# Kernel tuning notes

Measured on AMD Instinct MI355X. Metric: run time of the kernel, lower is better.

## Reference

```python
import jax, jax.numpy as jnp
import numpy as np

N_NODES = 20000
N_EDGES = 320000
N_GRAPHS = 16
NEG_SLOPE = 0.2


def gat_layer(x, src, dst, W, al, ar, b):
    # x: [N, F_in]; W: [F_in, H*D]; al/ar: [H, D]; b: [H*D]
    H, D = al.shape
    N = x.shape[0]
    f = (x @ W).reshape(N, H, D)                      # projected features [N,H,D]
    el = jnp.sum(f * al[None], axis=-1)                # [N,H]
    er = jnp.sum(f * ar[None], axis=-1)                # [N,H]
    e = jax.nn.leaky_relu(el[src] + er[dst], NEG_SLOPE)  # [E,H]
    # numerically stable segment softmax over incoming edges of each dst node
    m = jax.ops.segment_max(e, dst, num_segments=N)    # [N,H]
    m = jnp.where(jnp.isfinite(m), m, 0.0)
    ex = jnp.exp(e - m[dst])                           # [E,H]
    denom = jax.ops.segment_sum(ex, dst, num_segments=N)  # [N,H]
    msg = ex[:, :, None] * f[src]                      # [E,H,D]
    num = jax.ops.segment_sum(msg, dst, num_segments=N)   # [N,H,D]
    rst = num / jnp.where(denom > 0, denom, 1.0)[:, :, None]
    return rst + b.reshape(1, H, D)


def setup_inputs() -> dict:
    key = jax.random.key(0)
    ks = jax.random.split(key, 16)
    in_dim, hid, H = 128, 128, 3
    x = jax.random.normal(ks[0], (N_NODES, in_dim), dtype=jnp.float32)
    src = jax.random.randint(ks[1], (N_EDGES,), 0, N_NODES, dtype=jnp.int32)
    dst = jax.random.randint(ks[2], (N_EDGES,), 0, N_NODES, dtype=jnp.int32)
    graph_ids = jnp.sort(jax.random.randint(ks[3], (N_NODES,), 0, N_GRAPHS, dtype=jnp.int32))
    s = lambda d: 1.0 / np.sqrt(d)
    W1 = jax.random.normal(ks[4], (in_dim, H * hid), jnp.float32) * s(in_dim)
    al1 = jax.random.normal(ks[5], (H, hid), jnp.float32) * s(hid)
    ar1 = jax.random.normal(ks[6], (H, hid), jnp.float32) * s(hid)
    b1 = jnp.zeros((H * hid,), jnp.float32)
    W2 = jax.random.normal(ks[7], (H * hid, hid), jnp.float32) * s(H * hid)
    al2 = jax.random.normal(ks[8], (1, hid), jnp.float32) * s(hid)
    ar2 = jax.random.normal(ks[9], (1, hid), jnp.float32) * s(hid)
    b2 = jnp.zeros((hid,), jnp.float32)
    linW = jax.random.normal(ks[10], (hid, hid), jnp.float32) * s(hid)
    linb = jnp.zeros((hid,), jnp.float32)
    return dict(x=x, src=src, dst=dst, graph_ids=graph_ids, W1=W1, al1=al1,
                ar1=ar1, b1=b1, W2=W2, al2=al2, ar2=ar2, b2=b2, linW=linW, linb=linb)


def reference(x, src, dst, graph_ids, W1, al1, ar1, b1, W2, al2, ar2, b2, linW, linb):
    h = gat_layer(x, src, dst, W1, al1, ar1, b1)       # [N,3,hid]
    h = jax.nn.elu(h.reshape(h.shape[0], -1))          # [N,3*hid]
    h = gat_layer(h, src, dst, W2, al2, ar2, b2)       # [N,1,hid]
    h = h.squeeze(1)                                   # [N,hid]
    # dgl.mean_nodes over batched graph
    sums = jax.ops.segment_sum(h, graph_ids, num_segments=N_GRAPHS)      # [G,hid]
    cnts = jax.ops.segment_sum(jnp.ones_like(graph_ids, jnp.float32), graph_ids, num_segments=N_GRAPHS)
    hg = sums / jnp.maximum(cnts, 1.0)[:, None]
    return jax.nn.relu(hg @ linW + linb)
```

## Files before the change

kernel.cpp:

```cpp
#include <hip/hip_runtime.h>
#include <hip/hip_bf16.h>

#define NN 20000
#define NE 320000
#define NG 16
#define PSPLIT 32


__global__ void hist_kernel(const int* __restrict__ dst, int* __restrict__ indeg, int E) {
  int e = blockIdx.x * 256 + threadIdx.x;
  if (e < E) atomicAdd(&indeg[dst[e]], 1);
}

__global__ void exscan_kernel(const int* __restrict__ in, int* __restrict__ outp, int n) {
  __shared__ int wsum[16];
  __shared__ int wexcl[16];
  __shared__ int tot_s;
  __shared__ int carry_s;
  int t = threadIdx.x;
  int lane = t & 63, wv = t >> 6;
  if (t == 0) carry_s = 0;
  __syncthreads();
  for (int base = 0; base < n; base += 1024) {
    int i = base + t;
    int v = (i < n) ? in[i] : 0;
    int x = v;
#pragma unroll
    for (int off = 1; off < 64; off <<= 1) {
      int y = __shfl_up(x, off);
      if (lane >= off) x += y;
    }
    if (lane == 63) wsum[wv] = x;
    __syncthreads();
    int carry = carry_s;
    if (t < 16) {
      int s = wsum[t];
      int xs = s;
#pragma unroll
      for (int off = 1; off < 16; off <<= 1) {
        int y = __shfl_up(xs, off);
        if (t >= off) xs += y;
      }
      wexcl[t] = xs - s;
      if (t == 15) tot_s = xs;
    }
    __syncthreads();
    if (i < n) outp[i] = carry + wexcl[wv] + (x - v);
    if (t == 0) carry_s = carry + tot_s;
  }
  if (t == 0) outp[n] = carry_s;
}

__global__ void scatter_kernel(const int* __restrict__ src, const int* __restrict__ dst,
                               const int* __restrict__ rowptr, int* __restrict__ cursor,
                               int* __restrict__ csr_src, int E) {
  int e = blockIdx.x * 256 + threadIdx.x;
  if (e < E) {
    int d = dst[e];
    int p = atomicAdd(&cursor[d], 1);
    csr_src[rowptr[d] + p] = src[e];
  }
}


template <int K, int NFULL>
__launch_bounds__(256)
__global__ void gemm64_kernel(const float* __restrict__ A, const float* __restrict__ B,
                              float* __restrict__ C, int M) {
  __shared__ float As[64 * 36];
  __shared__ float Bs[32 * 128];
  int t = threadIdx.x;
  int m0 = blockIdx.x * 64;
  int n0 = blockIdx.y * 128;
  int tm = t >> 4, tn = t & 15;
  float acc[4][8];
#pragma unroll
  for (int i = 0; i < 4; i++)
#pragma unroll
    for (int j = 0; j < 8; j++) acc[i][j] = 0.f;

  for (int k0 = 0; k0 < K; k0 += 32) {
#pragma unroll
    for (int i = 0; i < 2; i++) {
      int idx = t + i * 256;
      int r = idx >> 3, kq = (idx & 7) * 4;
      int gm = m0 + r;
      float4 v = make_float4(0.f, 0.f, 0.f, 0.f);
      if (gm < M) v = *(const float4*)&A[(size_t)gm * K + k0 + kq];
      *(float4*)&As[r * 36 + kq] = v;
    }
#pragma unroll
    for (int i = 0; i < 4; i++) {
      int idx = t + i * 256;
      int kk = idx >> 5, nq = (idx & 31) * 4;
      float4 v = *(const float4*)&B[(size_t)(k0 + kk) * NFULL + n0 + nq];
      *(float4*)&Bs[kk * 128 + nq] = v;
    }
    __syncthreads();
#pragma unroll 8
    for (int k = 0; k < 32; k++) {
      float af[4];
#pragma unroll
      for (int i = 0; i < 4; i++) af[i] = As[(tm * 4 + i) * 36 + k];
      float4 b0 = *(const float4*)&Bs[k * 128 + tn * 4];
      float4 b1 = *(const float4*)&Bs[k * 128 + 64 + tn * 4];
      float bf[8] = {b0.x, b0.y, b0.z, b0.w, b1.x, b1.y, b1.z, b1.w};
#pragma unroll
      for (int i = 0; i < 4; i++)
#pragma unroll
        for (int j = 0; j < 8; j++) acc[i][j] += af[i] * bf[j];
    }
    __syncthreads();
  }
#pragma unroll
  for (int i = 0; i < 4; i++) {
    int gm = m0 + tm * 4 + i;
    if (gm < M) {
      *(float4*)&C[(size_t)gm * NFULL + n0 + tn * 4] =
          make_float4(acc[i][0], acc[i][1], acc[i][2], acc[i][3]);
      *(float4*)&C[(size_t)gm * NFULL + n0 + 64 + tn * 4] =
          make_float4(acc[i][4], acc[i][5], acc[i][6], acc[i][7]);
    }
  }
}


__global__ void att_coef_kernel(const float* __restrict__ f, const float* __restrict__ al,
                                const float* __restrict__ ar, float* __restrict__ el,
                                float* __restrict__ er, int NH, int H) {
  int w = (blockIdx.x * 256 + threadIdx.x) >> 6;
  int lane = threadIdx.x & 63;
  if (w >= NH) return;
  int h = w % H;
  const float* fr = f + (size_t)w * 128;
  float v0 = fr[lane], v1 = fr[64 + lane];
  float a0 = al[h * 128 + lane], a1 = al[h * 128 + 64 + lane];
  float r0 = ar[h * 128 + lane], r1 = ar[h * 128 + 64 + lane];
  float se = v0 * a0 + v1 * a1;
  float sr = v0 * r0 + v1 * r1;
  for (int off = 32; off; off >>= 1) {
    se += __shfl_down(se, off);
    sr += __shfl_down(sr, off);
  }
  if (lane == 0) { el[w] = se; er[w] = sr; }
}


__global__ void aggregate3_kernel(const float* __restrict__ f, const float* __restrict__ el,
                                  const float* __restrict__ er, const float* __restrict__ bias,
                                  const int* __restrict__ rowptr, const int* __restrict__ csr_src,
                                  float* __restrict__ out) {
  int n = blockIdx.x;
  int t = threadIdx.x;
  __shared__ float wbuf[3][128];
  __shared__ int sbuf[128];
  __shared__ float red[6];
  int rs = rowptr[n];
  int deg = rowptr[n + 1] - rs;
  float er0 = er[n * 3 + 0], er1 = er[n * 3 + 1], er2 = er[n * 3 + 2];
  float psum0 = 0.f, psum1 = 0.f, psum2 = 0.f;
  int h = t >> 5;
  int d = (t & 31) * 4;
  const float* fh = f + h * 128 + d;
  float4 acc = make_float4(0.f, 0.f, 0.f, 0.f);
  for (int base = 0; base < deg; base += 128) {
    int cnt = min(128, deg - base);
    if (t < cnt) {
      int s = csr_src[rs + base + t];
      sbuf[t] = s;
      float e0 = el[s * 3 + 0] + er0, e1 = el[s * 3 + 1] + er1, e2 = el[s * 3 + 2] + er2;
      e0 = e0 > 0.f ? e0 : 0.2f * e0;
      e1 = e1 > 0.f ? e1 : 0.2f * e1;
      e2 = e2 > 0.f ? e2 : 0.2f * e2;
      float w0 = __expf(e0), w1 = __expf(e1), w2 = __expf(e2);
      wbuf[0][t] = w0; wbuf[1][t] = w1; wbuf[2][t] = w2;
      psum0 += w0; psum1 += w1; psum2 += w2;
    }
    __syncthreads();
    if (t < 96) {
      int j = 0;
      for (; j + 4 <= cnt; j += 4) {
        int s0 = sbuf[j], s1 = sbuf[j + 1], s2 = sbuf[j + 2], s3 = sbuf[j + 3];
        float4 v0 = *(const float4*)(fh + (size_t)s0 * 384);
        float4 v1 = *(const float4*)(fh + (size_t)s1 * 384);
        float4 v2 = *(const float4*)(fh + (size_t)s2 * 384);
        float4 v3 = *(const float4*)(fh + (size_t)s3 * 384);
        float w0 = wbuf[h][j], w1 = wbuf[h][j + 1], w2 = wbuf[h][j + 2], w3 = wbuf[h][j + 3];
        acc.x += w0 * v0.x + w1 * v1.x + w2 * v2.x + w3 * v3.x;
        acc.y += w0 * v0.y + w1 * v1.y + w2 * v2.y + w3 * v3.y;
        acc.z += w0 * v0.z + w1 * v1.z + w2 * v2.z + w3 * v3.z;
        acc.w += w0 * v0.w + w1 * v1.w + w2 * v2.w + w3 * v3.w;
      }
      for (; j < cnt; j++) {
        int s = sbuf[j];
        float4 v = *(const float4*)(fh + (size_t)s * 384);
        float w = wbuf[h][j];
        acc.x += w * v.x; acc.y += w * v.y; acc.z += w * v.z; acc.w += w * v.w;
      }
    }
    __syncthreads();
  }
  for (int off = 32; off; off >>= 1) {
    psum0 += __shfl_down(psum0, off);
    psum1 += __shfl_down(psum1, off);
    psum2 += __shfl_down(psum2, off);
  }
  int wv = t >> 6, ln = t & 63;
  if (ln == 0) { red[wv * 3 + 0] = psum0; red[wv * 3 + 1] = psum1; red[wv * 3 + 2] = psum2; }
  __syncthreads();
  if (t < 96) {
    float dn = red[h] + red[3 + h];
    float inv = dn > 0.f ? 1.f / dn : 0.f;
    const float* bp = bias + h * 128 + d;
    float4 r;
    r.x = acc.x * inv + bp[0];
    r.y = acc.y * inv + bp[1];
    r.z = acc.z * inv + bp[2];
    r.w = acc.w * inv + bp[3];
    r.x = r.x > 0.f ? r.x : expm1f(r.x);
    r.y = r.y > 0.f ? r.y : expm1f(r.y);
    r.z = r.z > 0.f ? r.z : expm1f(r.z);
    r.w = r.w > 0.f ? r.w : expm1f(r.w);
    *(float4*)&out[(size_t)n * 384 + h * 128 + d] = r;
  }
}


__global__ void aggregate1_kernel(const float* __restrict__ f, const float* __restrict__ el,
                                  const float* __restrict__ er, const float* __restrict__ bias,
                                  const int* __restrict__ rowptr, const int* __restrict__ csr_src,
                                  float* __restrict__ out) {
  int n = blockIdx.x;
  int t = threadIdx.x;
  __shared__ float wbuf[128];
  __shared__ int sbuf[128];
  __shared__ float red[2];
  __shared__ float4 accbuf[4][32];
  int rs = rowptr[n];
  int deg = rowptr[n + 1] - rs;
  float ern = er[n];
  float psum = 0.f;
  int g = t >> 5;
  int d = (t & 31) * 4;
  const float* fd = f + d;
  float4 acc = make_float4(0.f, 0.f, 0.f, 0.f);
  for (int base = 0; base < deg; base += 128) {
    int cnt = min(128, deg - base);
    if (t < cnt) {
      int s = csr_src[rs + base + t];
      sbuf[t] = s;
      float e = el[s] + ern;
      e = e > 0.f ? e : 0.2f * e;
      float w = __expf(e);
      wbuf[t] = w;
      psum += w;
    }
    __syncthreads();
    int j = g;
    for (; j + 4 < cnt; j += 8) {
      int s0 = sbuf[j], s1 = sbuf[j + 4];
      float4 v0 = *(const float4*)(fd + (size_t)s0 * 128);
      float4 v1 = *(const float4*)(fd + (size_t)s1 * 128);
      float w0 = wbuf[j], w1 = wbuf[j + 4];
      acc.x += w0 * v0.x + w1 * v1.x;
      acc.y += w0 * v0.y + w1 * v1.y;
      acc.z += w0 * v0.z + w1 * v1.z;
      acc.w += w0 * v0.w + w1 * v1.w;
    }
    for (; j < cnt; j += 4) {
      int s = sbuf[j];
      float4 v = *(const float4*)(fd + (size_t)s * 128);
      float w = wbuf[j];
      acc.x += w * v.x; acc.y += w * v.y; acc.z += w * v.z; acc.w += w * v.w;
    }
    __syncthreads();
  }
  for (int off = 32; off; off >>= 1) psum += __shfl_down(psum, off);
  int wv = t >> 6, ln = t & 63;
  if (ln == 0) red[wv] = psum;
  accbuf[g][t & 31] = acc;
  __syncthreads();
  if (t < 32) {
    float4 a0 = accbuf[0][t], a1 = accbuf[1][t], a2 = accbuf[2][t], a3 = accbuf[3][t];
    float dn = red[0] + red[1];
    float inv = dn > 0.f ? 1.f / dn : 0.f;
    const float* bp = bias + t * 4;
    float4 r;
    r.x = (a0.x + a1.x + a2.x + a3.x) * inv + bp[0];
    r.y = (a0.y + a1.y + a2.y + a3.y) * inv + bp[1];
    r.z = (a0.z + a1.z + a2.z + a3.z) * inv + bp[2];
    r.w = (a0.w + a1.w + a2.w + a3.w) * inv + bp[3];
    *(float4*)&out[(size_t)n * 128 + t * 4] = r;
  }
}


__global__ void pool_partial_kernel(const float* __restrict__ h2, const int* __restrict__ gid,
                                    float* __restrict__ sums, int N) {
  int g = blockIdx.x / PSPLIT;
  int sp = blockIdx.x % PSPLIT;
  int tid = threadIdx.x;
  int lo0 = 0, hi0 = N;
  while (lo0 < hi0) { int m = (lo0 + hi0) >> 1; if (gid[m] < g) lo0 = m + 1; else hi0 = m; }
  int lo1 = lo0, hi1 = N;
  while (lo1 < hi1) { int m = (lo1 + hi1) >> 1; if (gid[m] < g + 1) lo1 = m + 1; else hi1 = m; }
  float a0 = 0.f, a1 = 0.f, a2 = 0.f, a3 = 0.f;
  int n = lo0 + sp;
  for (; n + 3 * PSPLIT < lo1; n += 4 * PSPLIT) {
    a0 += h2[(size_t)n * 128 + tid];
    a1 += h2[(size_t)(n + PSPLIT) * 128 + tid];
    a2 += h2[(size_t)(n + 2 * PSPLIT) * 128 + tid];
    a3 += h2[(size_t)(n + 3 * PSPLIT) * 128 + tid];
  }
  for (; n < lo1; n += PSPLIT) a0 += h2[(size_t)n * 128 + tid];
  float acc = (a0 + a1) + (a2 + a3);
  atomicAdd(&sums[g * 128 + tid], acc);
}

__global__ void pool_final_kernel(const float* __restrict__ sums, const int* __restrict__ gid,
                                  const float* __restrict__ linW, const float* __restrict__ linb,
                                  float* __restrict__ out, int N) {
  int g = blockIdx.x;
  int tid = threadIdx.x;
  int lo0 = 0, hi0 = N;
  while (lo0 < hi0) { int m = (lo0 + hi0) >> 1; if (gid[m] < g) lo0 = m + 1; else hi0 = m; }
  int lo1 = lo0, hi1 = N;
  while (lo1 < hi1) { int m = (lo1 + hi1) >> 1; if (gid[m] < g + 1) lo1 = m + 1; else hi1 = m; }
  int cnt = lo1 - lo0;
  float hg = sums[g * 128 + tid] / (float)(cnt > 0 ? cnt : 1);
  __shared__ float hgs[128];
  hgs[tid] = hg;
  __syncthreads();
  float o = linb[tid];
#pragma unroll 4
  for (int dd = 0; dd < 128; dd++) o += hgs[dd] * linW[dd * 128 + tid];
  out[g * 128 + tid] = fmaxf(o, 0.f);
}


extern "C" void kernel_launch(void* const* d_in, const int* in_sizes, int n_in,
                              void* d_out, int out_size, void* d_ws, size_t ws_size,
                              hipStream_t stream) {
  const float* x    = (const float*)d_in[0];
  const int*   src  = (const int*)d_in[1];
  const int*   dst  = (const int*)d_in[2];
  const int*   gid  = (const int*)d_in[3];
  const float* W1   = (const float*)d_in[4];
  const float* al1  = (const float*)d_in[5];
  const float* ar1  = (const float*)d_in[6];
  const float* b1   = (const float*)d_in[7];
  const float* W2   = (const float*)d_in[8];
  const float* al2  = (const float*)d_in[9];
  const float* ar2  = (const float*)d_in[10];
  const float* b2   = (const float*)d_in[11];
  const float* linW = (const float*)d_in[12];
  const float* linb = (const float*)d_in[13];
  float* out = (float*)d_out;

  char* ws = (char*)d_ws;
  size_t off = 0;
  auto alloc = [&](size_t bytes) -> void* {
    void* p = ws + off;
    off += (bytes + 255) & ~(size_t)255;
    return p;
  };
  float* f1      = (float*)alloc((size_t)NN * 384 * 4);
  float* h1      = (float*)alloc((size_t)NN * 384 * 4);
  float* f2      = (float*)alloc((size_t)NN * 128 * 4);
  float* h2      = (float*)alloc((size_t)NN * 128 * 4);
  float* el1     = (float*)alloc((size_t)NN * 3 * 4);
  float* er1     = (float*)alloc((size_t)NN * 3 * 4);
  float* el2     = (float*)alloc((size_t)NN * 4);
  float* er2     = (float*)alloc((size_t)NN * 4);
  int*   indeg   = (int*)alloc((size_t)NN * 4);
  int*   rowptr  = (int*)alloc((size_t)(NN + 1) * 4);
  int*   cursor  = (int*)alloc((size_t)NN * 4);
  int*   csr_src = (int*)alloc((size_t)NE * 4);
  float* gsums   = (float*)alloc((size_t)NG * 128 * 4);
  (void)ws_size;

  hipMemsetAsync(indeg, 0, (size_t)NN * 4, stream);
  hipMemsetAsync(cursor, 0, (size_t)NN * 4, stream);
  hipMemsetAsync(gsums, 0, (size_t)NG * 128 * 4, stream);

  hist_kernel<<<(NE + 255) / 256, 256, 0, stream>>>(dst, indeg, NE);
  exscan_kernel<<<1, 1024, 0, stream>>>(indeg, rowptr, NN);
  scatter_kernel<<<(NE + 255) / 256, 256, 0, stream>>>(src, dst, rowptr, cursor, csr_src, NE);

  gemm64_kernel<128, 384><<<dim3(313, 3), 256, 0, stream>>>(x, W1, f1, NN);
  att_coef_kernel<<<(NN * 3 + 3) / 4, 256, 0, stream>>>(f1, al1, ar1, el1, er1, NN * 3, 3);
  aggregate3_kernel<<<NN, 128, 0, stream>>>(f1, el1, er1, b1, rowptr, csr_src, h1);

  gemm64_kernel<384, 128><<<dim3(313, 1), 256, 0, stream>>>(h1, W2, f2, NN);
  att_coef_kernel<<<(NN + 3) / 4, 256, 0, stream>>>(f2, al2, ar2, el2, er2, NN, 1);
  aggregate1_kernel<<<NN, 128, 0, stream>>>(f2, el2, er2, b2, rowptr, csr_src, h2);

  pool_partial_kernel<<<NG * PSPLIT, 128, 0, stream>>>(h2, gid, gsums, NN);
  pool_final_kernel<<<NG, 128, 0, stream>>>(gsums, gid, linW, linb, out, NN);
}
```

Measured before the change: 340.1 us.

## Aggregate raw inputs before projection in first GAT layer via linearity

Layer one no longer gathers the projected 384-wide features per edge. It computes attention logits directly from x using precomputed W1·al and W1·ar vectors. It then aggregates the 128-wide raw x per head with softmax weights and applies W1 per head afterwards, with bias and ELU fused into the GEMM epilogue. This cuts per-edge gather traffic from 384 to 128 floats per edge and drops the f1 buffer and the first att_coef pass, at the cost of writing a 384-wide aggregated buffer and a batched per-head GEMM. The three memsets are also merged into one by reordering the workspace.

Result: faster. 316.0 us (-7.1%).

```diff
diff --git a/kernel.cpp b/kernel.cpp
--- a/kernel.cpp
+++ b/kernel.cpp
@@ -63,106 +63,61 @@
 }
 
 
-template <int K, int NFULL>
-__launch_bounds__(256)
-__global__ void gemm64_kernel(const float* __restrict__ A, const float* __restrict__ B,
-                              float* __restrict__ C, int M) {
-  __shared__ float As[64 * 36];
-  __shared__ float Bs[32 * 128];
+__global__ void prep_wlr_kernel(const float* __restrict__ W1, const float* __restrict__ al1,
+                                const float* __restrict__ ar1, float* __restrict__ wlr) {
+  int t = blockIdx.x * 256 + threadIdx.x;
+  if (t >= 768) return;
+  int k = t & 127;
+  int j = t >> 7;
+  int h = j % 3;
+  const float* av = (j < 3 ? al1 : ar1) + h * 128;
+  const float* wrow = W1 + (size_t)k * 384 + h * 128;
+  float s = 0.f;
+#pragma unroll 4
+  for (int d = 0; d < 128; d++) s += wrow[d] * av[d];
+  wlr[j * 128 + k] = s;
+}
+
+__global__ void elr_kernel(const float* __restrict__ x, const float* __restrict__ wlr,
+                           float* __restrict__ el, float* __restrict__ er, int N) {
+  __shared__ float wl_s[768];
   int t = threadIdx.x;
-  int m0 = blockIdx.x * 64;
-  int n0 = blockIdx.y * 128;
-  int tm = t >> 4, tn = t & 15;
-  float acc[4][8];
-#pragma unroll
-  for (int i = 0; i < 4; i++)
-#pragma unroll
-    for (int j = 0; j < 8; j++) acc[i][j] = 0.f;
-
-  for (int k0 = 0; k0 < K; k0 += 32) {
-#pragma unroll
-    for (int i = 0; i < 2; i++) {
-      int idx = t + i * 256;
-      int r = idx >> 3, kq = (idx & 7) * 4;
-      int gm = m0 + r;
-      float4 v = make_float4(0.f, 0.f, 0.f, 0.f);
-      if (gm < M) v = *(const float4*)&A[(size_t)gm * K + k0 + kq];
-      *(float4*)&As[r * 36 + kq] = v;
-    }
-#pragma unroll
-    for (int i = 0; i < 4; i++) {
-      int idx = t + i * 256;
-      int kk = idx >> 5, nq = (idx & 31) * 4;
-      float4 v = *(const float4*)&B[(size_t)(k0 + kk) * NFULL + n0 + nq];
-      *(float4*)&Bs[kk * 128 + nq] = v;
-    }
-    __syncthreads();
-#pragma unroll 8
-    for (int k = 0; k < 32; k++) {
-      float af[4];
-#pragma unroll
-      for (int i = 0; i < 4; i++) af[i] = As[(tm * 4 + i) * 36 + k];
-      float4 b0 = *(const float4*)&Bs[k * 128 + tn * 4];
-      float4 b1 = *(const float4*)&Bs[k * 128 + 64 + tn * 4];
-      float bf[8] = {b0.x, b0.y, b0.z, b0.w, b1.x, b1.y, b1.z, b1.w};
-#pragma unroll
-      for (int i = 0; i < 4; i++)
-#pragma unroll
-        for (int j = 0; j < 8; j++) acc[i][j] += af[i] * bf[j];
-    }
-    __syncthreads();
-  }
-#pragma unroll
-  for (int i = 0; i < 4; i++) {
-    int gm = m0 + tm * 4 + i;
-    if (gm < M) {
-      *(float4*)&C[(size_t)gm * NFULL + n0 + tn * 4] =
-          make_float4(acc[i][0], acc[i][1], acc[i][2], acc[i][3]);
-      *(float4*)&C[(size_t)gm * NFULL + n0 + 64 + tn * 4] =
-          make_float4(acc[i][4], acc[i][5], acc[i][6], acc[i][7]);
-    }
-  }
-}
-
-
-__global__ void att_coef_kernel(const float* __restrict__ f, const float* __restrict__ al,
-                                const float* __restrict__ ar, float* __restrict__ el,
-                                float* __restrict__ er, int NH, int H) {
-  int w = (blockIdx.x * 256 + threadIdx.x) >> 6;
-  int lane = threadIdx.x & 63;
-  if (w >= NH) return;
-  int h = w % H;
-  const float* fr = f + (size_t)w * 128;
-  float v0 = fr[lane], v1 = fr[64 + lane];
-  float a0 = al[h * 128 + lane], a1 = al[h * 128 + 64 + lane];
-  float r0 = ar[h * 128 + lane], r1 = ar[h * 128 + 64 + lane];
-  float se = v0 * a0 + v1 * a1;
-  float sr = v0 * r0 + v1 * r1;
-  for (int off = 32; off; off >>= 1) {
-    se += __shfl_down(se, off);
-    sr += __shfl_down(sr, off);
-  }
-  if (lane == 0) { el[w] = se; er[w] = sr; }
-}
-
-
-__global__ void aggregate3_kernel(const float* __restrict__ f, const float* __restrict__ el,
-                                  const float* __restrict__ er, const float* __restrict__ bias,
-                                  const int* __restrict__ rowptr, const int* __restrict__ csr_src,
-                                  float* __restrict__ out) {
+  for (int i = t; i < 768; i += 256) wl_s[i] = wlr[i];
+  __syncthreads();
+  int w = (blockIdx.x * 256 + t) >> 6;
+  int lane = t & 63;
+  if (w >= N) return;
+  float v0 = x[(size_t)w * 128 + lane], v1 = x[(size_t)w * 128 + 64 + lane];
+  float s[6];
+#pragma unroll
+  for (int j = 0; j < 6; j++) s[j] = v0 * wl_s[j * 128 + lane] + v1 * wl_s[j * 128 + 64 + lane];
+#pragma unroll
+  for (int off = 32; off; off >>= 1)
+#pragma unroll
+    for (int j = 0; j < 6; j++) s[j] += __shfl_down(s[j], off);
+  if (lane == 0) {
+    el[w * 3 + 0] = s[0]; el[w * 3 + 1] = s[1]; el[w * 3 + 2] = s[2];
+    er[w * 3 + 0] = s[3]; er[w * 3 + 1] = s[4]; er[w * 3 + 2] = s[5];
+  }
+}
+
+
+__global__ void aggregate_x_kernel(const float* __restrict__ x, const float* __restrict__ el,
+                                   const float* __restrict__ er, const int* __restrict__ rowptr,
+                                   const int* __restrict__ csr_src, float* __restrict__ aggx) {
   int n = blockIdx.x;
   int t = threadIdx.x;
   __shared__ float wbuf[3][128];
   __shared__ int sbuf[128];
   __shared__ float red[6];
+  __shared__ float4 accbuf[3][4][32];
   int rs = rowptr[n];
   int deg = rowptr[n + 1] - rs;
   float er0 = er[n * 3 + 0], er1 = er[n * 3 + 1], er2 = er[n * 3 + 2];
-  float psum0 = 0.f, psum1 = 0.f, psum2 = 0.f;
-  int h = t >> 5;
-  int d = (t & 31) * 4;
-  const float* fh = f + h * 128 + d;
-  float4 acc = make_float4(0.f, 0.f, 0.f, 0.f);
+  float p0 = 0.f, p1 = 0.f, p2 = 0.f;
+  int g = t >> 5, dq = t & 31;
+  const float* xd = x + dq * 4;
+  float4 a0 = make_float4(0, 0, 0, 0), a1 = a0, a2 = a0;
   for (int base = 0; base < deg; base += 128) {
     int cnt = min(128, deg - base);
     if (t < cnt) {
@@ -174,55 +129,155 @@
       e2 = e2 > 0.f ? e2 : 0.2f * e2;
       float w0 = __expf(e0), w1 = __expf(e1), w2 = __expf(e2);
       wbuf[0][t] = w0; wbuf[1][t] = w1; wbuf[2][t] = w2;
-      psum0 += w0; psum1 += w1; psum2 += w2;
-    }
-    __syncthreads();
-    if (t < 96) {
-      int j = 0;
-      for (; j + 4 <= cnt; j += 4) {
-        int s0 = sbuf[j], s1 = sbuf[j + 1], s2 = sbuf[j + 2], s3 = sbuf[j + 3];
-        float4 v0 = *(const float4*)(fh + (size_t)s0 * 384);
-        float4 v1 = *(const float4*)(fh + (size_t)s1 * 384);
-        float4 v2 = *(const float4*)(fh + (size_t)s2 * 384);
-        float4 v3 = *(const float4*)(fh + (size_t)s3 * 384);
-        float w0 = wbuf[h][j], w1 = wbuf[h][j + 1], w2 = wbuf[h][j + 2], w3 = wbuf[h][j + 3];
-        acc.x += w0 * v0.x + w1 * v1.x + w2 * v2.x + w3 * v3.x;
-        acc.y += w0 * v0.y + w1 * v1.y + w2 * v2.y + w3 * v3.y;
-        acc.z += w0 * v0.z + w1 * v1.z + w2 * v2.z + w3 * v3.z;
-        acc.w += w0 * v0.w + w1 * v1.w + w2 * v2.w + w3 * v3.w;
-      }
-      for (; j < cnt; j++) {
-        int s = sbuf[j];
-        float4 v = *(const float4*)(fh + (size_t)s * 384);
-        float w = wbuf[h][j];
-        acc.x += w * v.x; acc.y += w * v.y; acc.z += w * v.z; acc.w += w * v.w;
-      }
+      p0 += w0; p1 += w1; p2 += w2;
+    }
+    __syncthreads();
+    int j = g;
+    for (; j + 4 < cnt; j += 8) {
+      int s0 = sbuf[j], s1 = sbuf[j + 4];
+      float4 v0 = *(const float4*)(xd + (size_t)s0 * 128);
+      float4 v1 = *(const float4*)(xd + (size_t)s1 * 128);
+      float w00 = wbuf[0][j], w01 = wbuf[1][j], w02 = wbuf[2][j];
+      float w10 = wbuf[0][j + 4], w11 = wbuf[1][j + 4], w12 = wbuf[2][j + 4];
+      a0.x += w00 * v0.x + w10 * v1.x; a0.y += w00 * v0.y + w10 * v1.y;
+      a0.z += w00 * v0.z + w10 * v1.z; a0.w += w00 * v0.w + w10 * v1.w;
+      a1.x += w01 * v0.x + w11 * v1.x; a1.y += w01 * v0.y + w11 * v1.y;
+      a1.z += w01 * v0.z + w11 * v1.z; a1.w += w01 * v0.w + w11 * v1.w;
+      a2.x += w02 * v0.x + w12 * v1.x; a2.y += w02 * v0.y + w12 * v1.y;
+      a2.z += w02 * v0.z + w12 * v1.z; a2.w += w02 * v0.w + w12 * v1.w;
+    }
+    for (; j < cnt; j += 4) {
+      int s = sbuf[j];
+      float4 v = *(const float4*)(xd + (size_t)s * 128);
+      float w0 = wbuf[0][j], w1 = wbuf[1][j], w2 = wbuf[2][j];
+      a0.x += w0 * v.x; a0.y += w0 * v.y; a0.z += w0 * v.z; a0.w += w0 * v.w;
+      a1.x += w1 * v.x; a1.y += w1 * v.y; a1.z += w1 * v.z; a1.w += w1 * v.w;
+      a2.x += w2 * v.x; a2.y += w2 * v.y; a2.z += w2 * v.z; a2.w += w2 * v.w;
     }
     __syncthreads();
   }
   for (int off = 32; off; off >>= 1) {
-    psum0 += __shfl_down(psum0, off);
-    psum1 += __shfl_down(psum1, off);
-    psum2 += __shfl_down(psum2, off);
+    p0 += __shfl_down(p0, off);
+    p1 += __shfl_down(p1, off);
+    p2 += __shfl_down(p2, off);
   }
   int wv = t >> 6, ln = t & 63;
-  if (ln == 0) { red[wv * 3 + 0] = psum0; red[wv * 3 + 1] = psum1; red[wv * 3 + 2] = psum2; }
+  if (ln == 0) { red[wv * 3 + 0] = p0; red[wv * 3 + 1] = p1; red[wv * 3 + 2] = p2; }
+  accbuf[0][g][dq] = a0;
+  accbuf[1][g][dq] = a1;
+  accbuf[2][g][dq] = a2;
   __syncthreads();
   if (t < 96) {
+    int h = t >> 5, d = t & 31;
+    float4 s0 = accbuf[h][0][d], s1 = accbuf[h][1][d], s2 = accbuf[h][2][d], s3 = accbuf[h][3][d];
     float dn = red[h] + red[3 + h];
     float inv = dn > 0.f ? 1.f / dn : 0.f;
-    const float* bp = bias + h * 128 + d;
     float4 r;
-    r.x = acc.x * inv + bp[0];
-    r.y = acc.y * inv + bp[1];
-    r.z = acc.z * inv + bp[2];
-    r.w = acc.w * inv + bp[3];
-    r.x = r.x > 0.f ? r.x : expm1f(r.x);
-    r.y = r.y > 0.f ? r.y : expm1f(r.y);
-    r.z = r.z > 0.f ? r.z : expm1f(r.z);
-    r.w = r.w > 0.f ? r.w : expm1f(r.w);
-    *(float4*)&out[(size_t)n * 384 + h * 128 + d] = r;
-  }
+    r.x = (s0.x + s1.x + s2.x + s3.x) * inv;
+    r.y = (s0.y + s1.y + s2.y + s3.y) * inv;
+    r.z = (s0.z + s1.z + s2.z + s3.z) * inv;
+    r.w = (s0.w + s1.w + s2.w + s3.w) * inv;
+    *(float4*)&aggx[(size_t)n * 384 + h * 128 + d * 4] = r;
+  }
+}
+
+
+template <int K, bool BIAS_ELU>
+__launch_bounds__(256)
+__global__ void gemm64e_kernel(const float* __restrict__ A, int lda, int sA,
+                               const float* __restrict__ B, int ldb, int sB,
+                               float* __restrict__ C, int ldc, int sC,
+                               const float* __restrict__ bias, int sBias, int M) {
+  __shared__ float As[64 * 36];
+  __shared__ float Bs[32 * 128];
+  int hy = blockIdx.y;
+  A += (size_t)hy * sA; B += (size_t)hy * sB; C += (size_t)hy * sC;
+  if (BIAS_ELU) bias += (size_t)hy * sBias;
+  int t = threadIdx.x;
+  int m0 = blockIdx.x * 64;
+  int tm = t >> 4, tn = t & 15;
+  float acc[4][8];
+#pragma unroll
+  for (int i = 0; i < 4; i++)
+#pragma unroll
+    for (int j = 0; j < 8; j++) acc[i][j] = 0.f;
+
+  for (int k0 = 0; k0 < K; k0 += 32) {
+#pragma unroll
+    for (int i = 0; i < 2; i++) {
+      int idx = t + i * 256;
+      int r = idx >> 3, kq = (idx & 7) * 4;
+      int gm = m0 + r;
+      float4 v = make_float4(0.f, 0.f, 0.f, 0.f);
+      if (gm < M) v = *(const float4*)&A[(size_t)gm * lda + k0 + kq];
+      *(float4*)&As[r * 36 + kq] = v;
+    }
+#pragma unroll
+    for (int i = 0; i < 4; i++) {
+      int idx = t + i * 256;
+      int kk = idx >> 5, nq = (idx & 31) * 4;
+      float4 v = *(const float4*)&B[(size_t)(k0 + kk) * ldb + nq];
+      *(float4*)&Bs[kk * 128 + nq] = v;
+    }
+    __syncthreads();
+#pragma unroll 8
+    for (int k = 0; k < 32; k++) {
+      float af[4];
+#pragma unroll
+      for (int i = 0; i < 4; i++) af[i] = As[(tm * 4 + i) * 36 + k];
+      float4 b0 = *(const float4*)&Bs[k * 128 + tn * 4];
+      float4 b1 = *(const float4*)&Bs[k * 128 + 64 + tn * 4];
+      float bf[8] = {b0.x, b0.y, b0.z, b0.w, b1.x, b1.y, b1.z, b1.w};
+#pragma unroll
+      for (int i = 0; i < 4; i++)
+#pragma unroll
+        for (int j = 0; j < 8; j++) acc[i][j] += af[i] * bf[j];
+    }
+    __syncthreads();
+  }
+  float bv[8];
+  if (BIAS_ELU) {
+#pragma unroll
+    for (int j = 0; j < 4; j++) { bv[j] = bias[tn * 4 + j]; bv[4 + j] = bias[64 + tn * 4 + j]; }
+  }
+#pragma unroll
+  for (int i = 0; i < 4; i++) {
+    int gm = m0 + tm * 4 + i;
+    if (gm < M) {
+      float r[8];
+#pragma unroll
+      for (int j = 0; j < 8; j++) {
+        float v = acc[i][j];
+        if (BIAS_ELU) {
+          v += bv[j];
+          v = v > 0.f ? v : expm1f(v);
+        }
+        r[j] = v;
+      }
+      *(float4*)&C[(size_t)gm * ldc + tn * 4] = make_float4(r[0], r[1], r[2], r[3]);
+      *(float4*)&C[(size_t)gm * ldc + 64 + tn * 4] = make_float4(r[4], r[5], r[6], r[7]);
+    }
+  }
+}
+
+
+__global__ void att_coef_kernel(const float* __restrict__ f, const float* __restrict__ al,
+                                const float* __restrict__ ar, float* __restrict__ el,
+                                float* __restrict__ er, int NH) {
+  int w = (blockIdx.x * 256 + threadIdx.x) >> 6;
+  int lane = threadIdx.x & 63;
+  if (w >= NH) return;
+  const float* fr = f + (size_t)w * 128;
+  float v0 = fr[lane], v1 = fr[64 + lane];
+  float a0 = al[lane], a1 = al[64 + lane];
+  float r0 = ar[lane], r1 = ar[64 + lane];
+  float se = v0 * a0 + v1 * a1;
+  float sr = v0 * r0 + v1 * r1;
+  for (int off = 32; off; off >>= 1) {
+    se += __shfl_down(se, off);
+    sr += __shfl_down(sr, off);
+  }
+  if (lane == 0) { el[w] = se; er[w] = sr; }
 }
 
 
@@ -364,7 +419,7 @@
     off += (bytes + 255) & ~(size_t)255;
     return p;
   };
-  float* f1      = (float*)alloc((size_t)NN * 384 * 4);
+  float* aggx    = (float*)alloc((size_t)NN * 384 * 4);
   float* h1      = (float*)alloc((size_t)NN * 384 * 4);
   float* f2      = (float*)alloc((size_t)NN * 128 * 4);
   float* h2      = (float*)alloc((size_t)NN * 128 * 4);
@@ -372,27 +427,29 @@
   float* er1     = (float*)alloc((size_t)NN * 3 * 4);
   float* el2     = (float*)alloc((size_t)NN * 4);
   float* er2     = (float*)alloc((size_t)NN * 4);
+  float* wlr     = (float*)alloc((size_t)768 * 4);
+  int*   rowptr  = (int*)alloc((size_t)(NN + 1) * 4);
+  int*   csr_src = (int*)alloc((size_t)NE * 4);
   int*   indeg   = (int*)alloc((size_t)NN * 4);
-  int*   rowptr  = (int*)alloc((size_t)(NN + 1) * 4);
   int*   cursor  = (int*)alloc((size_t)NN * 4);
-  int*   csr_src = (int*)alloc((size_t)NE * 4);
   float* gsums   = (float*)alloc((size_t)NG * 128 * 4);
   (void)ws_size;
-
-  hipMemsetAsync(indeg, 0, (size_t)NN * 4, stream);
-  hipMemsetAsync(cursor, 0, (size_t)NN * 4, stream);
-  hipMemsetAsync(gsums, 0, (size_t)NG * 128 * 4, stream);
+  size_t zbytes = (char*)(gsums + NG * 128) - (char*)indeg;
+  hipMemsetAsync(indeg, 0, zbytes, stream);
 
   hist_kernel<<<(NE + 255) / 256, 256, 0, stream>>>(dst, indeg, NE);
   exscan_kernel<<<1, 1024, 0, stream>>>(indeg, rowptr, NN);
   scatter_kernel<<<(NE + 255) / 256, 256, 0, stream>>>(src, dst, rowptr, cursor, csr_src, NE);
 
-  gemm64_kernel<128, 384><<<dim3(313, 3), 256, 0, stream>>>(x, W1, f1, NN);
-  att_coef_kernel<<<(NN * 3 + 3) / 4, 256, 0, stream>>>(f1, al1, ar1, el1, er1, NN * 3, 3);
-  aggregate3_kernel<<<NN, 128, 0, stream>>>(f1, el1, er1, b1, rowptr, csr_src, h1);
-
-  gemm64_kernel<384, 128><<<dim3(313, 1), 256, 0, stream>>>(h1, W2, f2, NN);
-  att_coef_kernel<<<(NN + 3) / 4, 256, 0, stream>>>(f2, al2, ar2, el2, er2, NN, 1);
+  prep_wlr_kernel<<<3, 256, 0, stream>>>(W1, al1, ar1, wlr);
+  elr_kernel<<<(NN + 3) / 4, 256, 0, stream>>>(x, wlr, el1, er1, NN);
+  aggregate_x_kernel<<<NN, 128, 0, stream>>>(x, el1, er1, rowptr, csr_src, aggx);
+  gemm64e_kernel<128, true><<<dim3(313, 3), 256, 0, stream>>>(
+      aggx, 384, 128, W1, 384, 128, h1, 384, 128, b1, 128, NN);
+
+  gemm64e_kernel<384, false><<<dim3(313, 1), 256, 0, stream>>>(
+      h1, 384, 0, W2, 128, 0, f2, 128, 0, nullptr, 0, NN);
+  att_coef_kernel<<<(NN + 3) / 4, 256, 0, stream>>>(f2, al2, ar2, el2, er2, NN);
   aggregate1_kernel<<<NN, 128, 0, stream>>>(f2, el2, er2, b2, rowptr, csr_src, h2);
 
   pool_partial_kernel<<<NG * PSPLIT, 128, 0, stream>>>(h2, gid, gsums, NN);
```
